# Optimization experiments

Measured on AMD Instinct MI355X. Metric: run time of the kernel, lower is better.

## Reference

```python
import math
import jax, jax.numpy as jnp
import numpy as np

SQRT_HALF = math.sqrt(0.5)

def wn_linear(x, v, g, b):
    # weight_norm over dim=0 (default): W[o,:] = g[o] * v[o,:] / ||v[o,:]||
    w = v * (g / jnp.linalg.norm(v, axis=1))[:, None]
    return jnp.einsum('btc,ec->bte', x, w) + b

def setup_inputs() -> dict:
    key = jax.random.key(0)
    ks = jax.random.split(key, 7)
    B, T, S, C, E = 64, 1024, 1024, 512, 512
    return {
        'x': jax.random.normal(ks[0], (B, T, C), jnp.float32),
        'target_embedding': jax.random.normal(ks[1], (B, T, E), jnp.float32),
        'enc0': jax.random.normal(ks[2], (B, E, S), jnp.float32),
        'enc1': jax.random.normal(ks[3], (B, E, S), jnp.float32),
        'enc2': jax.random.normal(ks[4], (B, S, E), jnp.float32),
        'in_v': jax.random.normal(ks[5], (E, C), jnp.float32) * math.sqrt(1.0 / C),
        'in_g': jnp.ones((E,), jnp.float32),
        'in_b': jnp.zeros((E,), jnp.float32),
        'out_v': jax.random.normal(ks[6], (C, E), jnp.float32) * math.sqrt(1.0 / E),
        'out_g': jnp.ones((C,), jnp.float32),
        'out_b': jnp.zeros((C,), jnp.float32),
    }

def reference(x, target_embedding, enc0, enc1, enc2, in_v, in_g, in_b, out_v, out_g, out_b):
    residual = x
    h = (wn_linear(x, in_v, in_g, in_b) + target_embedding) * SQRT_HALF  # [B,T,E]
    scores = jnp.einsum('bte,bes->bts', h, enc0 + enc1)                  # [B,T,S]
    attn = jax.nn.softmax(scores, axis=-1)                               # softmax over S
    ctx = jnp.einsum('bts,bse->bte', attn, enc2)                         # [B,T,E]
    s = enc2.shape[1]
    ctx = ctx * (s * math.sqrt(1.0 / s))                                 # * sqrt(s)
    out = (wn_linear(ctx, out_v, out_g, out_b) + residual) * SQRT_HALF   # [B,T,C]
    return (out, attn)
```

## Files before the change

### kernel.cpp

```cpp
#include <hip/hip_runtime.h>
#include <hip/hip_fp16.h>

#define SQRT_HALF 0.70710678118654752f

typedef _Float16 f16x8 __attribute__((ext_vector_type(8)));
typedef _Float16 f16x4 __attribute__((ext_vector_type(4)));
typedef float    f32x4 __attribute__((ext_vector_type(4)));

#define B_ 64
#define T_ 1024
#define S_ 1024
#define C_ 512
#define E_ 512

#define BKK 64
#define LDK 72

template<int EPI, bool A_F16>
__launch_bounds__(256, 2)
__global__ void gemm_kernel(const void* __restrict__ Abase,
                            const _Float16* __restrict__ Bbase,
                            void* __restrict__ Dbase,
                            const float* __restrict__ bias,
                            const float* __restrict__ extra,
                            int K, long sA, long sB, long sD, int ldD)
{
    __shared__ _Float16 As[128 * LDK];
    __shared__ _Float16 Bs[128 * LDK];
    const int tid  = threadIdx.x;
    const int bz   = blockIdx.z;
    const int m0   = blockIdx.y * 128;
    const int n0   = blockIdx.x * 128;
    const int lane = tid & 63;
    const int wv   = tid >> 6;
    const int l15  = lane & 15;
    const int quad = lane >> 4;
    const int wm   = (wv >> 1) * 64;
    const int wn   = (wv & 1) * 64;

    f32x4 acc[4][4] = {};

    const _Float16* Bp = Bbase + bz * sB + (long)n0 * K;
    const _Float16* Ah = nullptr;
    const float*    Af = nullptr;
    if (A_F16) Ah = (const _Float16*)Abase + bz * sA + (long)m0 * K;
    else       Af = (const float*)Abase + bz * sA + (long)m0 * K;

    for (int k0 = 0; k0 < K; k0 += BKK) {
        if (A_F16) {
            #pragma unroll
            for (int it = 0; it < 4; ++it) {
                int idx = tid + it * 256;
                int r = idx >> 3, c8 = (idx & 7) << 3;
                *(uint4*)&As[r * LDK + c8] = *(const uint4*)(Ah + (long)r * K + k0 + c8);
            }
        } else {
            #pragma unroll
            for (int it = 0; it < 8; ++it) {
                int idx = tid + it * 256;
                int r = idx >> 4, c4 = (idx & 15) << 2;
                float4 v = *(const float4*)(Af + (long)r * K + k0 + c4);
                f16x4 hv;
                hv[0] = (_Float16)v.x; hv[1] = (_Float16)v.y;
                hv[2] = (_Float16)v.z; hv[3] = (_Float16)v.w;
                *(f16x4*)&As[r * LDK + c4] = hv;
            }
        }
        #pragma unroll
        for (int it = 0; it < 4; ++it) {
            int idx = tid + it * 256;
            int r = idx >> 3, c8 = (idx & 7) << 3;
            *(uint4*)&Bs[r * LDK + c8] = *(const uint4*)(Bp + (long)r * K + k0 + c8);
        }
        __syncthreads();
        #pragma unroll
        for (int kk = 0; kk < BKK; kk += 32) {
            f16x8 af[4], bf[4];
            #pragma unroll
            for (int mt = 0; mt < 4; ++mt)
                af[mt] = *(const f16x8*)&As[(wm + mt * 16 + l15) * LDK + kk + quad * 8];
            #pragma unroll
            for (int nt = 0; nt < 4; ++nt)
                bf[nt] = *(const f16x8*)&Bs[(wn + nt * 16 + l15) * LDK + kk + quad * 8];
            #pragma unroll
            for (int mt = 0; mt < 4; ++mt)
                #pragma unroll
                for (int nt = 0; nt < 4; ++nt)
                    acc[mt][nt] = __builtin_amdgcn_mfma_f32_16x16x32_f16(af[mt], bf[nt], acc[mt][nt], 0, 0, 0);
        }
        __syncthreads();
    }

    #pragma unroll
    for (int mt = 0; mt < 4; ++mt) {
        #pragma unroll
        for (int nt = 0; nt < 4; ++nt) {
            #pragma unroll
            for (int i = 0; i < 4; ++i) {
                int row = m0 + wm + mt * 16 + quad * 4 + i;
                int col = n0 + wn + nt * 16 + l15;
                float v = acc[mt][nt][i];
                long doff = bz * sD + (long)row * ldD + col;
                if constexpr (EPI == 0) {
                    v = (v + bias[col] + extra[(long)row * ldD + col]) * SQRT_HALF;
                    ((_Float16*)Dbase)[doff] = (_Float16)v;
                } else if constexpr (EPI == 1) {
                    ((float*)Dbase)[doff] = v;
                } else if constexpr (EPI == 2) {
                    ((_Float16*)Dbase)[doff] = (_Float16)(v * 32.0f);
                } else {
                    v = (v + bias[col] + extra[(long)row * ldD + col]) * SQRT_HALF;
                    ((float*)Dbase)[doff] = v;
                }
            }
        }
    }
}

__global__ void prep_kernel(const float* __restrict__ enc0, const float* __restrict__ enc1,
                            const float* __restrict__ enc2,
                            _Float16* __restrict__ KsumT, _Float16* __restrict__ enc2T)
{
    __shared__ float tk[32][33];
    __shared__ float t2[32][33];
    const int b  = blockIdx.z;
    const int e0 = blockIdx.y * 32;
    const int s0 = blockIdx.x * 32;
    const int t  = threadIdx.x;
    const int r  = t >> 5;
    const int c  = t & 31;

    const float* p0 = enc0 + ((long)b * E_ + e0) * S_ + s0;
    const float* p1 = enc1 + ((long)b * E_ + e0) * S_ + s0;
    const float* p2 = enc2 + ((long)b * S_ + s0) * E_ + e0;
    #pragma unroll
    for (int rr = 0; rr < 32; rr += 8) {
        tk[r + rr][c] = p0[(long)(r + rr) * S_ + c] + p1[(long)(r + rr) * S_ + c];
        t2[r + rr][c] = p2[(long)(r + rr) * E_ + c];
    }
    __syncthreads();
    _Float16* q1 = KsumT + ((long)b * S_ + s0) * E_ + e0;
    _Float16* q2 = enc2T + ((long)b * E_ + e0) * S_ + s0;
    #pragma unroll
    for (int rr = 0; rr < 32; rr += 8) {
        q1[(long)(r + rr) * E_ + c] = (_Float16)tk[c][r + rr];
        q2[(long)(r + rr) * S_ + c] = (_Float16)t2[c][r + rr];
    }
}

__global__ void weights_kernel(const float* __restrict__ in_v, const float* __restrict__ in_g,
                               const float* __restrict__ out_v, const float* __restrict__ out_g,
                               _Float16* __restrict__ w_in, _Float16* __restrict__ w_out)
{
    const int rowi = blockIdx.x;
    const float* v; const float* g; _Float16* w; int r;
    if (rowi < E_) { r = rowi;       v = in_v  + (long)r * C_; g = in_g;  w = w_in  + (long)r * C_; }
    else           { r = rowi - E_;  v = out_v + (long)r * E_; g = out_g; w = w_out + (long)r * E_; }
    const int t = threadIdx.x;
    float a = v[t], b2 = v[t + 256];
    float ss = a * a + b2 * b2;
    #pragma unroll
    for (int off = 32; off >= 1; off >>= 1) ss += __shfl_xor(ss, off, 64);
    __shared__ float red[4];
    if ((t & 63) == 0) red[t >> 6] = ss;
    __syncthreads();
    ss = red[0] + red[1] + red[2] + red[3];
    float scale = g[r] / sqrtf(ss);
    w[t]       = (_Float16)(a * scale);
    w[t + 256] = (_Float16)(b2 * scale);
}

__global__ void softmax_kernel(float* __restrict__ attn)
{
    const long row = blockIdx.x;
    float* p = attn + row * (long)S_;
    const int t = threadIdx.x;
    float4 v = *(float4*)(p + t * 4);
    float m = fmaxf(fmaxf(v.x, v.y), fmaxf(v.z, v.w));
    #pragma unroll
    for (int off = 32; off >= 1; off >>= 1) m = fmaxf(m, __shfl_xor(m, off, 64));
    __shared__ float redm[4], reds[4];
    if ((t & 63) == 0) redm[t >> 6] = m;
    __syncthreads();
    m = fmaxf(fmaxf(redm[0], redm[1]), fmaxf(redm[2], redm[3]));
    float e0 = __expf(v.x - m), e1 = __expf(v.y - m), e2 = __expf(v.z - m), e3 = __expf(v.w - m);
    float s = e0 + e1 + e2 + e3;
    #pragma unroll
    for (int off = 32; off >= 1; off >>= 1) s += __shfl_xor(s, off, 64);
    if ((t & 63) == 0) reds[t >> 6] = s;
    __syncthreads();
    s = reds[0] + reds[1] + reds[2] + reds[3];
    float inv = 1.0f / s;
    v.x = e0 * inv; v.y = e1 * inv; v.z = e2 * inv; v.w = e3 * inv;
    *(float4*)(p + t * 4) = v;
}

extern "C" void kernel_launch(void* const* d_in, const int* in_sizes, int n_in,
                              void* d_out, int out_size, void* d_ws, size_t ws_size,
                              hipStream_t stream)
{
    (void)in_sizes; (void)n_in; (void)out_size; (void)ws_size;
    const float* x     = (const float*)d_in[0];
    const float* te    = (const float*)d_in[1];
    const float* enc0  = (const float*)d_in[2];
    const float* enc1  = (const float*)d_in[3];
    const float* enc2  = (const float*)d_in[4];
    const float* in_v  = (const float*)d_in[5];
    const float* in_g  = (const float*)d_in[6];
    const float* in_b  = (const float*)d_in[7];
    const float* out_v = (const float*)d_in[8];
    const float* out_g = (const float*)d_in[9];
    const float* out_b = (const float*)d_in[10];

    float* out  = (float*)d_out;
    float* attn = out + (long)B_ * T_ * C_;

    _Float16* w_in  = (_Float16*)d_ws;
    _Float16* w_out = w_in  + (long)E_ * C_;
    _Float16* KsumT = w_out + (long)C_ * E_;
    _Float16* enc2T = KsumT + (long)B_ * S_ * E_;
    _Float16* hbuf  = enc2T + (long)B_ * E_ * S_;
    _Float16* ctxb  = hbuf  + (long)B_ * T_ * E_;

    prep_kernel<<<dim3(S_ / 32, E_ / 32, B_), 256, 0, stream>>>(enc0, enc1, enc2, KsumT, enc2T);
    weights_kernel<<<dim3(E_ + C_), 256, 0, stream>>>(in_v, in_g, out_v, out_g, w_in, w_out);
    gemm_kernel<0, false><<<dim3(E_ / 128, (B_ * T_) / 128, 1), 256, 0, stream>>>(
        x, w_in, hbuf, in_b, te, C_, 0, 0, 0, E_);
    gemm_kernel<1, true><<<dim3(S_ / 128, T_ / 128, B_), 256, 0, stream>>>(
        hbuf, KsumT, attn, nullptr, nullptr, E_,
        (long)T_ * E_, (long)S_ * E_, (long)T_ * S_, S_);
    softmax_kernel<<<dim3(B_ * T_), 256, 0, stream>>>(attn);
    gemm_kernel<2, false><<<dim3(E_ / 128, T_ / 128, B_), 256, 0, stream>>>(
        attn, enc2T, ctxb, nullptr, nullptr, S_,
        (long)T_ * S_, (long)E_ * S_, (long)T_ * E_, E_);
    gemm_kernel<3, true><<<dim3(C_ / 128, (B_ * T_) / 128, 1), 256, 0, stream>>>(
        ctxb, w_out, out, out_b, x, E_, 0, 0, 0, C_);
}
```

Before: 1.316 ms.

## Stage GEMM tiles with direct global-to-LDS loads and pre-cast fp32 operands to fp16

The GEMM kernel now loads both operand tiles straight from global memory into LDS with global_load_lds. This removes the register round-trip and the in-kernel fp32-to-fp16 conversion. To make every A operand fp16, a new cast kernel converts x up front, and softmax also writes an fp16 copy of attn for the context GEMM. Workspace buffers are aliased to fit the new arrays. In exchange the LDS row padding is dropped, which may cause bank conflicts on fragment reads, and the cast and extra fp16 write add separate memory passes.

```diff
diff --git a/kernel.cpp b/kernel.cpp
--- a/kernel.cpp
+++ b/kernel.cpp
@@ -14,19 +14,25 @@
 #define E_ 512
 
 #define BKK 64
-#define LDK 72
-
-template<int EPI, bool A_F16>
+
+__device__ __forceinline__ void gload16(const void* g, void* l)
+{
+    __builtin_amdgcn_global_load_lds(
+        (const __attribute__((address_space(1))) void*)g,
+        (__attribute__((address_space(3))) void*)l, 16, 0, 0);
+}
+
+template<int EPI>
 __launch_bounds__(256, 2)
-__global__ void gemm_kernel(const void* __restrict__ Abase,
+__global__ void gemm_kernel(const _Float16* __restrict__ Abase,
                             const _Float16* __restrict__ Bbase,
                             void* __restrict__ Dbase,
                             const float* __restrict__ bias,
                             const float* __restrict__ extra,
                             int K, long sA, long sB, long sD, int ldD)
 {
-    __shared__ _Float16 As[128 * LDK];
-    __shared__ _Float16 Bs[128 * LDK];
+    __shared__ _Float16 As[128 * BKK];
+    __shared__ _Float16 Bs[128 * BKK];
     const int tid  = threadIdx.x;
     const int bz   = blockIdx.z;
     const int m0   = blockIdx.y * 128;
@@ -40,37 +46,21 @@
 
     f32x4 acc[4][4] = {};
 
+    const _Float16* Ap = Abase + bz * sA + (long)m0 * K;
     const _Float16* Bp = Bbase + bz * sB + (long)n0 * K;
-    const _Float16* Ah = nullptr;
-    const float*    Af = nullptr;
-    if (A_F16) Ah = (const _Float16*)Abase + bz * sA + (long)m0 * K;
-    else       Af = (const float*)Abase + bz * sA + (long)m0 * K;
 
     for (int k0 = 0; k0 < K; k0 += BKK) {
-        if (A_F16) {
-            #pragma unroll
-            for (int it = 0; it < 4; ++it) {
-                int idx = tid + it * 256;
-                int r = idx >> 3, c8 = (idx & 7) << 3;
-                *(uint4*)&As[r * LDK + c8] = *(const uint4*)(Ah + (long)r * K + k0 + c8);
-            }
-        } else {
-            #pragma unroll
-            for (int it = 0; it < 8; ++it) {
-                int idx = tid + it * 256;
-                int r = idx >> 4, c4 = (idx & 15) << 2;
-                float4 v = *(const float4*)(Af + (long)r * K + k0 + c4);
-                f16x4 hv;
-                hv[0] = (_Float16)v.x; hv[1] = (_Float16)v.y;
-                hv[2] = (_Float16)v.z; hv[3] = (_Float16)v.w;
-                *(f16x4*)&As[r * LDK + c4] = hv;
-            }
-        }
         #pragma unroll
         for (int it = 0; it < 4; ++it) {
             int idx = tid + it * 256;
-            int r = idx >> 3, c8 = (idx & 7) << 3;
-            *(uint4*)&Bs[r * LDK + c8] = *(const uint4*)(Bp + (long)r * K + k0 + c8);
+            int r = idx >> 3, c = (idx & 7) << 3;
+            gload16(Ap + (long)r * K + k0 + c, &As[idx * 8]);
+        }
+        #pragma unroll
+        for (int it = 0; it < 4; ++it) {
+            int idx = tid + it * 256;
+            int r = idx >> 3, c = (idx & 7) << 3;
+            gload16(Bp + (long)r * K + k0 + c, &Bs[idx * 8]);
         }
         __syncthreads();
         #pragma unroll
@@ -78,10 +68,10 @@
             f16x8 af[4], bf[4];
             #pragma unroll
             for (int mt = 0; mt < 4; ++mt)
-                af[mt] = *(const f16x8*)&As[(wm + mt * 16 + l15) * LDK + kk + quad * 8];
+                af[mt] = *(const f16x8*)&As[(wm + mt * 16 + l15) * BKK + kk + quad * 8];
             #pragma unroll
             for (int nt = 0; nt < 4; ++nt)
-                bf[nt] = *(const f16x8*)&Bs[(wn + nt * 16 + l15) * LDK + kk + quad * 8];
+                bf[nt] = *(const f16x8*)&Bs[(wn + nt * 16 + l15) * BKK + kk + quad * 8];
             #pragma unroll
             for (int mt = 0; mt < 4; ++mt)
                 #pragma unroll
@@ -148,6 +138,17 @@
     }
 }
 
+__global__ void cast_kernel(const float* __restrict__ src, _Float16* __restrict__ dst)
+{
+    long i = (((long)blockIdx.x * 256) + threadIdx.x) * 8;
+    float4 a = *(const float4*)(src + i);
+    float4 b = *(const float4*)(src + i + 4);
+    f16x8 h;
+    h[0] = (_Float16)a.x; h[1] = (_Float16)a.y; h[2] = (_Float16)a.z; h[3] = (_Float16)a.w;
+    h[4] = (_Float16)b.x; h[5] = (_Float16)b.y; h[6] = (_Float16)b.z; h[7] = (_Float16)b.w;
+    *(f16x8*)(dst + i) = h;
+}
+
 __global__ void weights_kernel(const float* __restrict__ in_v, const float* __restrict__ in_g,
                                const float* __restrict__ out_v, const float* __restrict__ out_g,
                                _Float16* __restrict__ w_in, _Float16* __restrict__ w_out)
@@ -170,10 +171,11 @@
     w[t + 256] = (_Float16)(b2 * scale);
 }
 
-__global__ void softmax_kernel(float* __restrict__ attn)
+__global__ void softmax_kernel(float* __restrict__ attn, _Float16* __restrict__ attnh)
 {
     const long row = blockIdx.x;
     float* p = attn + row * (long)S_;
+    _Float16* ph = attnh + row * (long)S_;
     const int t = threadIdx.x;
     float4 v = *(float4*)(p + t * 4);
     float m = fmaxf(fmaxf(v.x, v.y), fmaxf(v.z, v.w));
@@ -193,6 +195,9 @@
     float inv = 1.0f / s;
     v.x = e0 * inv; v.y = e1 * inv; v.z = e2 * inv; v.w = e3 * inv;
     *(float4*)(p + t * 4) = v;
+    f16x4 h;
+    h[0] = (_Float16)v.x; h[1] = (_Float16)v.y; h[2] = (_Float16)v.z; h[3] = (_Float16)v.w;
+    *(f16x4*)(ph + t * 4) = h;
 }
 
 extern "C" void kernel_launch(void* const* d_in, const int* in_sizes, int n_in,
@@ -219,20 +224,23 @@
     _Float16* w_out = w_in  + (long)E_ * C_;
     _Float16* KsumT = w_out + (long)C_ * E_;
     _Float16* enc2T = KsumT + (long)B_ * S_ * E_;
-    _Float16* hbuf  = enc2T + (long)B_ * E_ * S_;
-    _Float16* ctxb  = hbuf  + (long)B_ * T_ * E_;
+    _Float16* xh    = enc2T + (long)B_ * E_ * S_;
+    _Float16* hbuf  = xh    + (long)B_ * T_ * C_;
+    _Float16* attnh = xh;
+    _Float16* ctxb  = KsumT;
 
     prep_kernel<<<dim3(S_ / 32, E_ / 32, B_), 256, 0, stream>>>(enc0, enc1, enc2, KsumT, enc2T);
     weights_kernel<<<dim3(E_ + C_), 256, 0, stream>>>(in_v, in_g, out_v, out_g, w_in, w_out);
-    gemm_kernel<0, false><<<dim3(E_ / 128, (B_ * T_) / 128, 1), 256, 0, stream>>>(
-        x, w_in, hbuf, in_b, te, C_, 0, 0, 0, E_);
-    gemm_kernel<1, true><<<dim3(S_ / 128, T_ / 128, B_), 256, 0, stream>>>(
+    cast_kernel<<<dim3((B_ * T_ * C_) / (256 * 8)), 256, 0, stream>>>(x, xh);
+    gemm_kernel<0><<<dim3(E_ / 128, (B_ * T_) / 128, 1), 256, 0, stream>>>(
+        xh, w_in, hbuf, in_b, te, C_, 0, 0, 0, E_);
+    gemm_kernel<1><<<dim3(S_ / 128, T_ / 128, B_), 256, 0, stream>>>(
         hbuf, KsumT, attn, nullptr, nullptr, E_,
         (long)T_ * E_, (long)S_ * E_, (long)T_ * S_, S_);
-    softmax_kernel<<<dim3(B_ * T_), 256, 0, stream>>>(attn);
-    gemm_kernel<2, false><<<dim3(E_ / 128, T_ / 128, B_), 256, 0, stream>>>(
-        attn, enc2T, ctxb, nullptr, nullptr, S_,
+    softmax_kernel<<<dim3(B_ * T_), 256, 0, stream>>>(attn, attnh);
+    gemm_kernel<2><<<dim3(E_ / 128, T_ / 128, B_), 256, 0, stream>>>(
+        attnh, enc2T, ctxb, nullptr, nullptr, S_,
         (long)T_ * S_, (long)E_ * S_, (long)T_ * E_, E_);
-    gemm_kernel<3, true><<<dim3(C_ / 128, (B_ * T_) / 128, 1), 256, 0, stream>>>(
+    gemm_kernel<3><<<dim3(C_ / 128, (B_ * T_) / 128, 1), 256, 0, stream>>>(
         ctxb, w_out, out, out_b, x, E_, 0, 0, 0, C_);
 }
```

Measured after the change: 1.286 ms. -2.2%, faster.
